# Kernel tuning notes

Hardware: AMD Instinct MI355X
Metric: run time of the kernel (lower is better)

The kernel has to match this reference:

```python
import jax, jax.numpy as jnp
import numpy as np

B, S, D, H, F = 2, 2048, 3072, 32, 8192
DH = D // H  # 96
EPS = 1e-5


def setup_inputs() -> dict:
    key = jax.random.key(0)
    ks = jax.random.split(key, 16)
    sd = 0.02
    inp = {
        "hidden_states": jax.random.normal(ks[0], (B, S, D), jnp.float32),
        "ln1_g": jnp.ones((D,), jnp.float32),
        "ln1_b": jnp.zeros((D,), jnp.float32),
        "Wq": jax.random.normal(ks[1], (D, H, DH), jnp.float32) * sd,
        "bq": jnp.zeros((H, DH), jnp.float32),
        "Wk": jax.random.normal(ks[2], (D, H, DH), jnp.float32) * sd,
        "bk": jnp.zeros((H, DH), jnp.float32),
        "Wv": jax.random.normal(ks[3], (D, H, DH), jnp.float32) * sd,
        "bv": jnp.zeros((H, DH), jnp.float32),
        "Wo": jax.random.normal(ks[4], (H, DH, D), jnp.float32) * sd,
        "bo": jnp.zeros((D,), jnp.float32),
        "ln2_g": jnp.ones((D,), jnp.float32),
        "ln2_b": jnp.zeros((D,), jnp.float32),
        "W1": jax.random.normal(ks[5], (D, F), jnp.float32) * sd,
        "b1": jnp.zeros((F,), jnp.float32),
        "W2": jax.random.normal(ks[6], (F, D), jnp.float32) * sd,
        "b2": jnp.zeros((D,), jnp.float32),
    }
    return inp


def _layernorm(x, g, b):
    m = jnp.mean(x, axis=-1, keepdims=True)
    v = jnp.mean(jnp.square(x - m), axis=-1, keepdims=True)
    return (x - m) * jax.lax.rsqrt(v + EPS) * g + b


def reference(hidden_states, ln1_g, ln1_b, Wq, bq, Wk, bk, Wv, bv, Wo, bo,
              ln2_g, ln2_b, W1, b1, W2, b2):
    # --- LN + self-attention + residual ---
    h = _layernorm(hidden_states, ln1_g, ln1_b)  # [B,S,D]
    q = jnp.einsum('bsd,dhk->bshk', h, Wq) + bq  # [B,S,H,DH]
    k = jnp.einsum('bsd,dhk->bshk', h, Wk) + bk
    v = jnp.einsum('bsd,dhk->bshk', h, Wv) + bv
    scale = 1.0 / np.sqrt(DH).astype(np.float32)
    scores = jnp.einsum('bshk,bthk->bhst', q, k) * scale  # [B,H,S,S]
    attn = jax.nn.softmax(scores, axis=-1)
    ctx = jnp.einsum('bhst,bthk->bshk', attn, v)  # [B,S,H,DH]
    attn_out = jnp.einsum('bshk,hkd->bsd', ctx, Wo) + bo
    h1 = hidden_states + attn_out
    # --- LN + MLP + residual ---
    h2 = _layernorm(h1, ln2_g, ln2_b)
    mlp = jax.nn.gelu(h2 @ W1 + b1, approximate=False) @ W2 + b2
    return h1 + mlp
```

## Files before the change

### kernel.cpp

```cpp
#include <hip/hip_runtime.h>
#include <math.h>

#define DEV __device__ __forceinline__

typedef __attribute__((ext_vector_type(8))) __bf16 bfrag;
typedef __attribute__((ext_vector_type(4))) float f4;
typedef __attribute__((ext_vector_type(8))) unsigned short u16x8;
typedef __attribute__((ext_vector_type(4))) unsigned short u16x4;

DEV unsigned short f2bf(float f) {
  __bf16 b = (__bf16)f;
  unsigned short u;
  __builtin_memcpy(&u, &b, 2);
  return u;
}

DEV void gload_lds16(const void* g, void* l) {
  __builtin_amdgcn_global_load_lds((const __attribute__((address_space(1))) void*)g,
                                   (__attribute__((address_space(3))) void*)l, 16, 0, 0);
}

template<int EPI, int OUTBF, int BIASROW>
__global__ __launch_bounds__(256, 2)
void gemm_bt(const unsigned short* __restrict__ A,
             const unsigned short* __restrict__ Bt,
             const float* __restrict__ bias,
             const float* __restrict__ res,
             void* __restrict__ outp,
             int M, int N, int K, int gm, int cm, int cn)
{
  __shared__ unsigned short As[2][128 * 32];
  __shared__ unsigned short Bs[2][128 * 32];
  const int tid = threadIdx.x;
  const int lane = tid & 63;
  const int wid = tid >> 6;
  const int wr = wid >> 1, wc = wid & 1;
  const int l15 = lane & 15, lg = lane >> 4;

  const int xcd = blockIdx.x & 7, bidx = blockIdx.x >> 3;
  const int cgm = gm / cm;
  const int tm = (xcd % cgm) * cm + bidx % cm;
  const int tn = (xcd / cgm) * cn + bidx / cm;
  const long tM = (long)tm * 128;
  const long tN = (long)tn * 128;

  const int c0 = tid, c1 = tid + 256;
  const int r0 = c0 >> 2, k0 = (c0 & 3) * 8;
  const int r1 = c1 >> 2, k1 = (c1 & 3) * 8;

  const unsigned short* A0 = A + (tM + r0) * (long)K + k0;
  const unsigned short* A1 = A + (tM + r1) * (long)K + k1;
  const unsigned short* B0 = Bt + (tN + r0) * (long)K + k0;
  const unsigned short* B1 = Bt + (tN + r1) * (long)K + k1;

  auto stage = [&](int kt, int buf) {
    const long ko = (long)kt * 32;
    gload_lds16(A0 + ko, &As[buf][c0 * 8]);
    gload_lds16(A1 + ko, &As[buf][c1 * 8]);
    gload_lds16(B0 + ko, &Bs[buf][c0 * 8]);
    gload_lds16(B1 + ko, &Bs[buf][c1 * 8]);
  };

  stage(0, 0);
  f4 acc[4][4] = {};
  const int nk = K >> 5;
  int cur = 0;
  __syncthreads();
  for (int kt = 0; kt < nk; ++kt) {
    if (kt + 1 < nk) stage(kt + 1, cur ^ 1);
    bfrag aF[4], bF[4];
#pragma unroll
    for (int m = 0; m < 4; ++m)
      aF[m] = *(const bfrag*)&As[cur][(wr * 64 + m * 16 + l15) * 32 + lg * 8];
#pragma unroll
    for (int n = 0; n < 4; ++n)
      bF[n] = *(const bfrag*)&Bs[cur][(wc * 64 + n * 16 + l15) * 32 + lg * 8];
#pragma unroll
    for (int m = 0; m < 4; ++m)
#pragma unroll
      for (int n = 0; n < 4; ++n)
        acc[m][n] = __builtin_amdgcn_mfma_f32_16x16x32_bf16(aF[m], bF[n], acc[m][n], 0, 0, 0);
    __syncthreads();
    cur ^= 1;
  }

#pragma unroll
  for (int m = 0; m < 4; ++m) {
#pragma unroll
    for (int n = 0; n < 4; ++n) {
      const long col = tN + wc * 64 + n * 16 + l15;
      const float bcol = BIASROW ? 0.f : bias[col];
#pragma unroll
      for (int e = 0; e < 4; ++e) {
        const long row = tM + wr * 64 + m * 16 + lg * 4 + e;
        float v = acc[m][n][e] + (BIASROW ? bias[row] : bcol);
        if constexpr (EPI == 1) v = 0.5f * v * (1.0f + erff(v * 0.70710678118654752f));
        if constexpr (EPI == 2) v += res[row * N + col];
        if constexpr (OUTBF) ((unsigned short*)outp)[row * N + col] = f2bf(v);
        else                 ((float*)outp)[row * N + col] = v;
      }
    }
  }
}

template<int EPI, int OUTBF, int BIASROW>
__global__ __launch_bounds__(512, 2)
void gemm256(const unsigned short* __restrict__ A,
             const unsigned short* __restrict__ Bt,
             const float* __restrict__ bias,
             const float* __restrict__ res,
             void* __restrict__ outp,
             int M, int N, int K, int gm, int cm, int cn)
{
  __shared__ unsigned short As[2][256 * 64];
  __shared__ unsigned short Bs[2][256 * 64];

  const int tid = threadIdx.x;
  const int lane = tid & 63;
  const int wid = tid >> 6;
  const int wm = wid >> 2, wn = wid & 3;
  const int l15 = lane & 15, lg = lane >> 4;

  const int xcd = blockIdx.x & 7, bidx = blockIdx.x >> 3;
  const int cgm = gm / cm;
  const int tm = (xcd % cgm) * cm + bidx % cm;
  const int tn = (xcd / cgm) * cn + bidx / cm;
  const long tM = (long)tm * 256, tN = (long)tn * 256;

  const int srow = tid >> 3;
  const int lslot = (tid & 7) ^ (srow & 7);
  const unsigned short* aSrc = A + (tM + srow) * (long)K + lslot * 8;
  const unsigned short* bSrc = Bt + (tN + srow) * (long)K + lslot * 8;
  const int NT = K >> 6;

  auto stA = [&](int t, int j) {
    gload_lds16(aSrc + (long)t * 64 + (long)j * 64 * K, &As[t & 1][j * 4096 + tid * 8]);
  };
  auto stB = [&](int t, int j) {
    gload_lds16(bSrc + (long)t * 64 + (long)j * 64 * K, &Bs[t & 1][j * 4096 + tid * 8]);
  };

#pragma unroll
  for (int j = 0; j < 4; ++j) stA(0, j);
#pragma unroll
  for (int j = 0; j < 4; ++j) stB(0, j);
  stA(1, 0); stA(1, 2);
#pragma unroll
  for (int j = 0; j < 4; ++j) stB(1, j);
  asm volatile("s_waitcnt vmcnt(6)" ::: "memory");
  __builtin_amdgcn_s_barrier();

  const int aRow = (wm * 128 + l15) * 64;
  const int bRow = (wn * 64 + l15) * 64;
  const int sx = l15 & 7;
  const int sl0 = ((0 + lg) ^ sx) * 8;
  const int sl1 = ((4 + lg) ^ sx) * 8;

  bfrag aL[4][2], aH[4][2], b01[2][2], b23[2][2];
  f4 acc[8][4] = {};

  int cur = 0;
  for (int t = 0; t < NT; ++t, cur ^= 1) {
    const unsigned short* Ac = As[cur];
    const unsigned short* Bc = Bs[cur];
    const bool s1 = (t + 1 < NT);
    const bool s2 = (t + 2 < NT);

#pragma unroll
    for (int m = 0; m < 4; ++m) {
      aL[m][0] = *(const bfrag*)&Ac[aRow + m * 1024 + sl0];
      aL[m][1] = *(const bfrag*)&Ac[aRow + m * 1024 + sl1];
    }
#pragma unroll
    for (int n = 0; n < 2; ++n) {
      b01[n][0] = *(const bfrag*)&Bc[bRow + n * 1024 + sl0];
      b01[n][1] = *(const bfrag*)&Bc[bRow + n * 1024 + sl1];
    }
#pragma unroll
    for (int n = 0; n < 2; ++n) {
      b23[n][0] = *(const bfrag*)&Bc[bRow + (n + 2) * 1024 + sl0];
      b23[n][1] = *(const bfrag*)&Bc[bRow + (n + 2) * 1024 + sl1];
    }
    if (s1) { stA(t + 1, 1); stA(t + 1, 3); }
    __builtin_amdgcn_s_barrier();
    __builtin_amdgcn_s_setprio(1);
#pragma unroll
    for (int m = 0; m < 4; ++m)
#pragma unroll
      for (int n = 0; n < 2; ++n) {
        acc[m][n] = __builtin_amdgcn_mfma_f32_16x16x32_bf16(aL[m][0], b01[n][0], acc[m][n], 0, 0, 0);
        acc[m][n] = __builtin_amdgcn_mfma_f32_16x16x32_bf16(aL[m][1], b01[n][1], acc[m][n], 0, 0, 0);
      }
    __builtin_amdgcn_s_setprio(0);
    __builtin_amdgcn_s_barrier();

#pragma unroll
    for (int m = 0; m < 4; ++m) {
      aH[m][0] = *(const bfrag*)&Ac[aRow + 4096 + m * 1024 + sl0];
      aH[m][1] = *(const bfrag*)&Ac[aRow + 4096 + m * 1024 + sl1];
    }
    if (s2) { stA(t + 2, 0); stA(t + 2, 2); }
    __builtin_amdgcn_s_barrier();
    __builtin_amdgcn_s_setprio(1);
#pragma unroll
    for (int m = 0; m < 4; ++m)
#pragma unroll
      for (int n = 0; n < 2; ++n) {
        acc[m][2 + n] = __builtin_amdgcn_mfma_f32_16x16x32_bf16(aL[m][0], b23[n][0], acc[m][2 + n], 0, 0, 0);
        acc[m][2 + n] = __builtin_amdgcn_mfma_f32_16x16x32_bf16(aL[m][1], b23[n][1], acc[m][2 + n], 0, 0, 0);
      }
    __builtin_amdgcn_s_setprio(0);
    __builtin_amdgcn_s_barrier();

    if (s2) { stB(t + 2, 0); stB(t + 2, 1); }
    __builtin_amdgcn_s_barrier();
    __builtin_amdgcn_s_setprio(1);
#pragma unroll
    for (int m = 0; m < 4; ++m)
#pragma unroll
      for (int n = 0; n < 2; ++n) {
        acc[4 + m][2 + n] = __builtin_amdgcn_mfma_f32_16x16x32_bf16(aH[m][0], b23[n][0], acc[4 + m][2 + n], 0, 0, 0);
        acc[4 + m][2 + n] = __builtin_amdgcn_mfma_f32_16x16x32_bf16(aH[m][1], b23[n][1], acc[4 + m][2 + n], 0, 0, 0);
      }
    __builtin_amdgcn_s_setprio(0);
    __builtin_amdgcn_s_barrier();

    if (s2) { stB(t + 2, 2); stB(t + 2, 3); }
    __builtin_amdgcn_s_setprio(1);
#pragma unroll
    for (int m = 0; m < 4; ++m)
#pragma unroll
      for (int n = 0; n < 2; ++n) {
        acc[4 + m][n] = __builtin_amdgcn_mfma_f32_16x16x32_bf16(aH[m][0], b01[n][0], acc[4 + m][n], 0, 0, 0);
        acc[4 + m][n] = __builtin_amdgcn_mfma_f32_16x16x32_bf16(aH[m][1], b01[n][1], acc[4 + m][n], 0, 0, 0);
      }
    __builtin_amdgcn_s_setprio(0);
    if (s2)      asm volatile("s_waitcnt vmcnt(6)" ::: "memory");
    else if (s1) asm volatile("s_waitcnt vmcnt(0)" ::: "memory");
    __builtin_amdgcn_s_barrier();
  }

#pragma unroll
  for (int m = 0; m < 8; ++m) {
    const long row0 = tM + wm * 128 + m * 16 + lg * 4;
#pragma unroll
    for (int n = 0; n < 4; ++n) {
      const long col = tN + wn * 64 + n * 16 + l15;
      const float bc = BIASROW ? 0.f : bias[col];
#pragma unroll
      for (int e = 0; e < 4; ++e) {
        const long row = row0 + e;
        float v = acc[m][n][e] + (BIASROW ? bias[row] : bc);
        if constexpr (EPI == 1) v = 0.5f * v * (1.0f + erff(v * 0.70710678118654752f));
        if constexpr (EPI == 2) v += res[row * N + col];
        if constexpr (OUTBF) ((unsigned short*)outp)[row * N + col] = f2bf(v);
        else                 ((float*)outp)[row * N + col] = v;
      }
    }
  }
}

__global__ __launch_bounds__(256)
void ln_bf16(const float* __restrict__ x, const float* __restrict__ g,
             const float* __restrict__ b, unsigned short* __restrict__ out)
{
  __shared__ float red[4];
  const int tid = threadIdx.x;
  const long row = blockIdx.x;
  const float* xr = x + row * 3072;
  float4 v[3];
  float s = 0.f;
#pragma unroll
  for (int i = 0; i < 3; ++i) {
    v[i] = *(const float4*)&xr[i * 1024 + tid * 4];
    s += v[i].x + v[i].y + v[i].z + v[i].w;
  }
#pragma unroll
  for (int o = 32; o > 0; o >>= 1) s += __shfl_xor(s, o);
  if ((tid & 63) == 0) red[tid >> 6] = s;
  __syncthreads();
  s = red[0] + red[1] + red[2] + red[3];
  const float mean = s * (1.f / 3072.f);
  float vs = 0.f;
#pragma unroll
  for (int i = 0; i < 3; ++i) {
    const float dx = v[i].x - mean, dy = v[i].y - mean;
    const float dz = v[i].z - mean, dw = v[i].w - mean;
    vs += dx * dx + dy * dy + dz * dz + dw * dw;
  }
#pragma unroll
  for (int o = 32; o > 0; o >>= 1) vs += __shfl_xor(vs, o);
  __syncthreads();
  if ((tid & 63) == 0) red[tid >> 6] = vs;
  __syncthreads();
  vs = red[0] + red[1] + red[2] + red[3];
  const float rstd = rsqrtf(vs * (1.f / 3072.f) + 1e-5f);
#pragma unroll
  for (int i = 0; i < 3; ++i) {
    const int idx = i * 1024 + tid * 4;
    const float* vp = (const float*)&v[i];
    u16x4 o4;
#pragma unroll
    for (int c = 0; c < 4; ++c)
      o4[c] = f2bf((vp[c] - mean) * rstd * g[idx + c] + b[idx + c]);
    *(u16x4*)&out[row * 3072 + idx] = o4;
  }
}

__global__ __launch_bounds__(256)
void prep_weights(const float* __restrict__ Wq, const float* __restrict__ Wk,
                  const float* __restrict__ Wv, const float* __restrict__ Wo,
                  const float* __restrict__ W1, const float* __restrict__ W2,
                  const float* __restrict__ bq, const float* __restrict__ bk,
                  unsigned short* __restrict__ WqkT, unsigned short* __restrict__ WvT,
                  unsigned short* __restrict__ WoT, unsigned short* __restrict__ W1T,
                  unsigned short* __restrict__ W2T, float* __restrict__ bqk)
{
  __shared__ float tile[64][65];
  const int tid = threadIdx.x;
  int bid = blockIdx.x;
  if (bid < 24) {
    const int i = bid * 256 + tid;
    bqk[i] = (i < 3072) ? bq[i] : bk[i - 3072];
    return;
  }
  bid -= 24;
  const float* in; unsigned short* out; int R, C, nbx;
  if (bid < 2304)       { in = Wq; out = WqkT;               R = 3072; C = 3072; nbx = 48; }
  else if (bid < 4608)  { in = Wk; out = WqkT + 3072 * 3072; R = 3072; C = 3072; nbx = 48; bid -= 2304; }
  else if (bid < 6912)  { in = Wv; out = WvT;                R = 3072; C = 3072; nbx = 48; bid -= 4608; }
  else if (bid < 9216)  { in = Wo; out = WoT;                R = 3072; C = 3072; nbx = 48; bid -= 6912; }
  else if (bid < 15360) { in = W1; out = W1T;                R = 3072; C = 8192; nbx = 128; bid -= 9216; }
  else                  { in = W2; out = W2T;                R = 8192; C = 3072; nbx = 48; bid -= 15360; }
  const int bx = bid % nbx, by = bid / nbx;
  const long r0 = (long)by * 64, c0 = (long)bx * 64;
  const int tr = tid >> 4;
  const int tc = (tid & 15) * 4;

#pragma unroll
  for (int p = 0; p < 4; ++p) {
    const int row = p * 16 + tr;
    const float4 v = *(const float4*)&in[(r0 + row) * C + c0 + tc];
    tile[row][tc + 0] = v.x; tile[row][tc + 1] = v.y;
    tile[row][tc + 2] = v.z; tile[row][tc + 3] = v.w;
  }
  __syncthreads();

#pragma unroll
  for (int q = 0; q < 4; ++q) {
    const int c = q * 16 + tr;
    u16x4 o4;
#pragma unroll
    for (int j = 0; j < 4; ++j)
      o4[j] = f2bf(tile[tc + j][c]);
    *(u16x4*)&out[(c0 + c) * R + r0 + tc] = o4;
  }
}

__global__ __launch_bounds__(256, 4)
void attn_fwd(const unsigned short* __restrict__ qk,
              const unsigned short* __restrict__ vT,
              unsigned short* __restrict__ ctx)
{
  __shared__ unsigned short Ks[64 * 104];
  __shared__ unsigned short Vt[96 * 72];
  __shared__ unsigned short Ps[4 * 16 * 72];
  const int tid = threadIdx.x;
  const int lane = tid & 63;
  const int w = tid >> 6;
  const int l15 = lane & 15, lg = lane >> 4;
  const int bid = (blockIdx.x & 7) * 256 + (blockIdx.x >> 3);
  const int qb = bid & 31;
  const int h = (bid >> 5) & 31;
  const int b = bid >> 10;
  const long qkbase = ((long)b * 2048) * 6144 + h * 96;
  const long obase  = ((long)b * 2048) * 3072 + h * 96;
  const long vbase  = (long)(h * 96) * 4096 + (long)b * 2048;
  const int qbase = qb * 64;

  bfrag qf[3];
#pragma unroll
  for (int ks = 0; ks < 3; ++ks)
    qf[ks] = *(const bfrag*)&qk[qkbase + (long)(qbase + w * 16 + l15) * 6144 + ks * 32 + lg * 8];

  const int kr0 = tid / 12,         kk0 = (tid % 12) * 8;
  const int kr1 = (tid + 256) / 12, kk1 = ((tid + 256) % 12) * 8;
  const int kr2 = (tid + 512) / 12, kk2 = ((tid + 512) % 12) * 8;
  const unsigned short* kg = qk + qkbase + 3072;
  const int vd0 = tid >> 3,           vk0 = (tid & 7) * 8;
  const int vd1 = (tid + 256) >> 3,   vk1 = ((tid + 256) & 7) * 8;
  const int vd2 = (tid + 512) >> 3,   vk2 = ((tid + 512) & 7) * 8;
  const unsigned short* vg = vT + vbase;

  u16x8 kA = *(const u16x8*)&kg[(long)kr0 * 6144 + kk0];
  u16x8 kB = *(const u16x8*)&kg[(long)kr1 * 6144 + kk1];
  u16x8 kC = *(const u16x8*)&kg[(long)kr2 * 6144 + kk2];
  u16x8 vA = *(const u16x8*)&vg[(long)vd0 * 4096 + vk0];
  u16x8 vB = *(const u16x8*)&vg[(long)vd1 * 4096 + vk1];
  u16x8 vC = *(const u16x8*)&vg[(long)vd2 * 4096 + vk2];

  float m_run = -1e30f, l_run = 0.f;
  f4 O[6] = {};
  const float sc = 0.1020620726f * 1.4426950409f;

  for (int t = 0; t < 32; ++t) {
    *(u16x8*)&Ks[kr0 * 104 + kk0] = kA;
    *(u16x8*)&Ks[kr1 * 104 + kk1] = kB;
    *(u16x8*)&Ks[kr2 * 104 + kk2] = kC;
    *(u16x8*)&Vt[vd0 * 72 + vk0] = vA;
    *(u16x8*)&Vt[vd1 * 72 + vk1] = vB;
    *(u16x8*)&Vt[vd2 * 72 + vk2] = vC;
    __syncthreads();
    if (t + 1 < 32) {
      const long ko = (long)(t + 1) * 64 * 6144;
      const long vo = (long)(t + 1) * 64;
      kA = *(const u16x8*)&kg[ko + (long)kr0 * 6144 + kk0];
      kB = *(const u16x8*)&kg[ko + (long)kr1 * 6144 + kk1];
      kC = *(const u16x8*)&kg[ko + (long)kr2 * 6144 + kk2];
      vA = *(const u16x8*)&vg[vo + (long)vd0 * 4096 + vk0];
      vB = *(const u16x8*)&vg[vo + (long)vd1 * 4096 + vk1];
      vC = *(const u16x8*)&vg[vo + (long)vd2 * 4096 + vk2];
    }

    f4 sf[4];
#pragma unroll
    for (int mb = 0; mb < 4; ++mb) {
      f4 z = {0.f, 0.f, 0.f, 0.f};
      sf[mb] = z;
#pragma unroll
      for (int ks = 0; ks < 3; ++ks) {
        bfrag kf = *(const bfrag*)&Ks[(mb * 16 + l15) * 104 + ks * 32 + lg * 8];
        sf[mb] = __builtin_amdgcn_mfma_f32_16x16x32_bf16(kf, qf[ks], sf[mb], 0, 0, 0);
      }
    }
    float p[16];
    float tmax = -1e30f;
#pragma unroll
    for (int mb = 0; mb < 4; ++mb)
#pragma unroll
      for (int e = 0; e < 4; ++e) {
        const float sv = sf[mb][e] * sc;
        p[mb * 4 + e] = sv;
        tmax = fmaxf(tmax, sv);
      }
    tmax = fmaxf(tmax, __shfl_xor(tmax, 16));
    tmax = fmaxf(tmax, __shfl_xor(tmax, 32));
    const bool noskip = !__all(tmax - m_run <= 8.0f);
    float mnew = m_run, alpha = 1.0f;
    if (noskip) {
      mnew = fmaxf(m_run, tmax);
      alpha = exp2f(m_run - mnew);
    }
    float psum = 0.f;
#pragma unroll
    for (int i = 0; i < 16; ++i) {
      p[i] = exp2f(p[i] - mnew);
      psum += p[i];
    }
    psum += __shfl_xor(psum, 16);
    psum += __shfl_xor(psum, 32);
    l_run = l_run * alpha + psum;
    m_run = mnew;
#pragma unroll
    for (int mb = 0; mb < 4; ++mb) {
      u16x4 pw;
#pragma unroll
      for (int e = 0; e < 4; ++e) pw[e] = f2bf(p[mb * 4 + e]);
      *(u16x4*)&Ps[w * 1152 + l15 * 72 + mb * 16 + lg * 4] = pw;
    }
    if (noskip) {
      float aE[4];
#pragma unroll
      for (int e = 0; e < 4; ++e) aE[e] = __shfl(alpha, lg * 4 + e);
#pragma unroll
      for (int nb = 0; nb < 6; ++nb)
#pragma unroll
        for (int e = 0; e < 4; ++e) O[nb][e] *= aE[e];
    }
    bfrag pf[2];
#pragma unroll
    for (int ks = 0; ks < 2; ++ks)
      pf[ks] = *(const bfrag*)&Ps[w * 1152 + l15 * 72 + ks * 32 + lg * 8];
#pragma unroll
    for (int nb = 0; nb < 6; ++nb)
#pragma unroll
      for (int ks = 0; ks < 2; ++ks) {
        bfrag vf = *(const bfrag*)&Vt[(nb * 16 + l15) * 72 + ks * 32 + lg * 8];
        O[nb] = __builtin_amdgcn_mfma_f32_16x16x32_bf16(pf[ks], vf, O[nb], 0, 0, 0);
      }
    __syncthreads();
  }
  float lE[4];
#pragma unroll
  for (int e = 0; e < 4; ++e) lE[e] = 1.f / __shfl(l_run, lg * 4 + e);
#pragma unroll
  for (int nb = 0; nb < 6; ++nb)
#pragma unroll
    for (int e = 0; e < 4; ++e) {
      const long row = qbase + w * 16 + lg * 4 + e;
      ctx[obase + row * 3072 + nb * 16 + l15] = f2bf(O[nb][e] * lE[e]);
    }
}

extern "C" void kernel_launch(void* const* d_in, const int* in_sizes, int n_in,
                              void* d_out, int out_size, void* d_ws, size_t ws_size,
                              hipStream_t stream)
{
  (void)in_sizes; (void)n_in; (void)out_size; (void)ws_size;
  const float* x    = (const float*)d_in[0];
  const float* ln1g = (const float*)d_in[1];
  const float* ln1b = (const float*)d_in[2];
  const float* Wq   = (const float*)d_in[3];
  const float* bq   = (const float*)d_in[4];
  const float* Wk   = (const float*)d_in[5];
  const float* bk   = (const float*)d_in[6];
  const float* Wv   = (const float*)d_in[7];
  const float* bv   = (const float*)d_in[8];
  const float* Wo   = (const float*)d_in[9];
  const float* bo   = (const float*)d_in[10];
  const float* ln2g = (const float*)d_in[11];
  const float* ln2b = (const float*)d_in[12];
  const float* W1   = (const float*)d_in[13];
  const float* b1   = (const float*)d_in[14];
  const float* W2   = (const float*)d_in[15];
  const float* b2   = (const float*)d_in[16];

  char* ws = (char*)d_ws;
  unsigned short* WqkT = (unsigned short*)(ws + 0);
  unsigned short* WvT  = (unsigned short*)(ws + 37748736);
  unsigned short* WoT  = (unsigned short*)(ws + 56623104);
  unsigned short* W1T  = (unsigned short*)(ws + 75497472);
  unsigned short* W2T  = (unsigned short*)(ws + 125829120);
  float*          bqk  = (float*)(ws + 176160768);
  unsigned short* hbf  = (unsigned short*)(ws + 176185344);
  unsigned short* ctxb = hbf;
  unsigned short* qkb  = (unsigned short*)(ws + 201351168);
  unsigned short* h2   = qkb;
  unsigned short* act  = (unsigned short*)(ws + 251682816);
  unsigned short* vTb  = (unsigned short*)(ws + 318791680);
  float*          h1   = (float*)d_out;

  const dim3 blk(256);
  const dim3 blk512(512);

  prep_weights<<<24 + 21504, blk, 0, stream>>>(Wq, Wk, Wv, Wo, W1, W2, bq, bk,
                                               WqkT, WvT, WoT, W1T, W2T, bqk);

  ln_bf16<<<4096, blk, 0, stream>>>(x, ln1g, ln1b, hbf);

  gemm256<0, 1, 0><<<384, blk512, 0, stream>>>(hbf, WqkT, bqk, nullptr, qkb, 4096, 6144, 3072, 16, 8, 6);
  gemm256<0, 1, 1><<<192, blk512, 0, stream>>>(WvT, hbf, bv, nullptr, vTb, 3072, 4096, 3072, 12, 6, 4);

  attn_fwd<<<2048, blk, 0, stream>>>(qkb, vTb, ctxb);

  gemm256<2, 0, 0><<<192, blk512, 0, stream>>>(ctxb, WoT, bo, x, h1, 4096, 3072, 3072, 16, 4, 6);

  ln_bf16<<<4096, blk, 0, stream>>>(h1, ln2g, ln2b, h2);

  gemm256<1, 1, 0><<<512, blk512, 0, stream>>>(h2, W1T, b1, nullptr, act, 4096, 8192, 3072, 16, 8, 8);
  gemm_bt<2, 0, 0><<<768, blk, 0, stream>>>(act, W2T, b2, h1, (float*)d_out, 4096, 3072, 8192, 32, 16, 6);
}
```

Baseline: 1.168 ms.

## Split K in two for the W2 GEMM and accumulate with atomics

The final MLP down-projection GEMM (K=8192) now splits K across two halves of a doubled grid. Each half accumulates into the fp32 output with atomicAdd, and only the first half adds the bias. The launch-bounds occupancy hint for this kernel rises from 2 to 4 blocks per CU. The aim is more parallel work and better latency hiding on a long-K GEMM, at the cost of atomic traffic. The residual is no longer added explicitly, so correctness depends on the output buffer already holding h1.

```diff
diff --git a/kernel.cpp b/kernel.cpp
--- a/kernel.cpp
+++ b/kernel.cpp
@@ -21,13 +21,13 @@
 }
 
 template<int EPI, int OUTBF, int BIASROW>
-__global__ __launch_bounds__(256, 2)
+__global__ __launch_bounds__(256, 4)
 void gemm_bt(const unsigned short* __restrict__ A,
              const unsigned short* __restrict__ Bt,
              const float* __restrict__ bias,
              const float* __restrict__ res,
              void* __restrict__ outp,
-             int M, int N, int K, int gm, int cm, int cn)
+             int M, int N, int K, int gm, int cm, int cn, int nsplit)
 {
   __shared__ unsigned short As[2][128 * 32];
   __shared__ unsigned short Bs[2][128 * 32];
@@ -37,7 +37,13 @@
   const int wr = wid >> 1, wc = wid & 1;
   const int l15 = lane & 15, lg = lane >> 4;
 
-  const int xcd = blockIdx.x & 7, bidx = blockIdx.x >> 3;
+  const int half = gridDim.x >> 1;
+  const int kh = (nsplit == 2 && (int)blockIdx.x >= half) ? 1 : 0;
+  const int bxid = blockIdx.x - kh * half;
+  const int ksub = K / nsplit;
+  const long koff = (long)kh * ksub;
+
+  const int xcd = bxid & 7, bidx = bxid >> 3;
   const int cgm = gm / cm;
   const int tm = (xcd % cgm) * cm + bidx % cm;
   const int tn = (xcd / cgm) * cn + bidx / cm;
@@ -48,10 +54,10 @@
   const int r0 = c0 >> 2, k0 = (c0 & 3) * 8;
   const int r1 = c1 >> 2, k1 = (c1 & 3) * 8;
 
-  const unsigned short* A0 = A + (tM + r0) * (long)K + k0;
-  const unsigned short* A1 = A + (tM + r1) * (long)K + k1;
-  const unsigned short* B0 = Bt + (tN + r0) * (long)K + k0;
-  const unsigned short* B1 = Bt + (tN + r1) * (long)K + k1;
+  const unsigned short* A0 = A + (tM + r0) * (long)K + koff + k0;
+  const unsigned short* A1 = A + (tM + r1) * (long)K + koff + k1;
+  const unsigned short* B0 = Bt + (tN + r0) * (long)K + koff + k0;
+  const unsigned short* B1 = Bt + (tN + r1) * (long)K + koff + k1;
 
   auto stage = [&](int kt, int buf) {
     const long ko = (long)kt * 32;
@@ -63,7 +69,7 @@
 
   stage(0, 0);
   f4 acc[4][4] = {};
-  const int nk = K >> 5;
+  const int nk = ksub >> 5;
   int cur = 0;
   __syncthreads();
   for (int kt = 0; kt < nk; ++kt) {
@@ -93,11 +99,17 @@
 #pragma unroll
       for (int e = 0; e < 4; ++e) {
         const long row = tM + wr * 64 + m * 16 + lg * 4 + e;
-        float v = acc[m][n][e] + (BIASROW ? bias[row] : bcol);
-        if constexpr (EPI == 1) v = 0.5f * v * (1.0f + erff(v * 0.70710678118654752f));
-        if constexpr (EPI == 2) v += res[row * N + col];
-        if constexpr (OUTBF) ((unsigned short*)outp)[row * N + col] = f2bf(v);
-        else                 ((float*)outp)[row * N + col] = v;
+        float v = acc[m][n][e];
+        if constexpr (EPI == 3) {
+          if (kh == 0) v += (BIASROW ? bias[row] : bcol);
+          atomicAdd(&((float*)outp)[row * N + col], v);
+        } else {
+          v += (BIASROW ? bias[row] : bcol);
+          if constexpr (EPI == 1) v = 0.5f * v * (1.0f + erff(v * 0.70710678118654752f));
+          if constexpr (EPI == 2) v += res[row * N + col];
+          if constexpr (OUTBF) ((unsigned short*)outp)[row * N + col] = f2bf(v);
+          else                 ((float*)outp)[row * N + col] = v;
+        }
       }
     }
   }
@@ -558,5 +570,6 @@
   ln_bf16<<<4096, blk, 0, stream>>>(h1, ln2g, ln2b, h2);
 
   gemm256<1, 1, 0><<<512, blk512, 0, stream>>>(h2, W1T, b1, nullptr, act, 4096, 8192, 3072, 16, 8, 8);
-  gemm_bt<2, 0, 0><<<768, blk, 0, stream>>>(act, W2T, b2, h1, (float*)d_out, 4096, 3072, 8192, 32, 16, 6);
-}
+  gemm_bt<3, 0, 0><<<1536, blk, 0, stream>>>(act, W2T, b2, nullptr, (float*)d_out,
+                                             4096, 3072, 8192, 32, 16, 6, 2);
+}
```

Measured after the change: 1.212 ms. 1.04x slower.

## Double attention query tile to 128 rows with 512-thread blocks

Applied to the files above, without the earlier changes.

The attention kernel now processes 128 query rows per block using 8 waves instead of 64 rows with 4 waves, halving the grid. Each K/V tile loaded into shared memory is reused by twice as many query rows, which halves global K/V traffic. Load work is redistributed so 512 threads cover the 768 chunks, with only half the threads doing a second load. Larger blocks may reduce occupancy and make the wave distribution across CUs less even.

```diff
diff --git a/kernel.cpp b/kernel.cpp
--- a/kernel.cpp
+++ b/kernel.cpp
@@ -357,69 +357,70 @@
   }
 }
 
-__global__ __launch_bounds__(256, 4)
+__global__ __launch_bounds__(512, 4)
 void attn_fwd(const unsigned short* __restrict__ qk,
               const unsigned short* __restrict__ vT,
               unsigned short* __restrict__ ctx)
 {
   __shared__ unsigned short Ks[64 * 104];
   __shared__ unsigned short Vt[96 * 72];
-  __shared__ unsigned short Ps[4 * 16 * 72];
+  __shared__ unsigned short Ps[8 * 16 * 72];
   const int tid = threadIdx.x;
   const int lane = tid & 63;
   const int w = tid >> 6;
   const int l15 = lane & 15, lg = lane >> 4;
-  const int bid = (blockIdx.x & 7) * 256 + (blockIdx.x >> 3);
-  const int qb = bid & 31;
-  const int h = (bid >> 5) & 31;
-  const int b = bid >> 10;
+  const int bid = (blockIdx.x & 7) * 128 + (blockIdx.x >> 3);
+  const int qb = bid & 15;
+  const int h = (bid >> 4) & 31;
+  const int b = bid >> 9;
   const long qkbase = ((long)b * 2048) * 6144 + h * 96;
   const long obase  = ((long)b * 2048) * 3072 + h * 96;
   const long vbase  = (long)(h * 96) * 4096 + (long)b * 2048;
-  const int qbase = qb * 64;
+  const int qbase = qb * 128;
 
   bfrag qf[3];
 #pragma unroll
   for (int ks = 0; ks < 3; ++ks)
     qf[ks] = *(const bfrag*)&qk[qkbase + (long)(qbase + w * 16 + l15) * 6144 + ks * 32 + lg * 8];
 
-  const int kr0 = tid / 12,         kk0 = (tid % 12) * 8;
-  const int kr1 = (tid + 256) / 12, kk1 = ((tid + 256) % 12) * 8;
-  const int kr2 = (tid + 512) / 12, kk2 = ((tid + 512) % 12) * 8;
+  const bool two = (w < 4);
+  const int kcA = tid, kcB = tid + 512;
+  const int krA = kcA / 12, kkA = (kcA % 12) * 8;
+  const int krB = kcB / 12, kkB = (kcB % 12) * 8;
   const unsigned short* kg = qk + qkbase + 3072;
-  const int vd0 = tid >> 3,           vk0 = (tid & 7) * 8;
-  const int vd1 = (tid + 256) >> 3,   vk1 = ((tid + 256) & 7) * 8;
-  const int vd2 = (tid + 512) >> 3,   vk2 = ((tid + 512) & 7) * 8;
+  const int vdA = kcA >> 3, vkA = (kcA & 7) * 8;
+  const int vdB = kcB >> 3, vkB = (kcB & 7) * 8;
   const unsigned short* vg = vT + vbase;
 
-  u16x8 kA = *(const u16x8*)&kg[(long)kr0 * 6144 + kk0];
-  u16x8 kB = *(const u16x8*)&kg[(long)kr1 * 6144 + kk1];
-  u16x8 kC = *(const u16x8*)&kg[(long)kr2 * 6144 + kk2];
-  u16x8 vA = *(const u16x8*)&vg[(long)vd0 * 4096 + vk0];
-  u16x8 vB = *(const u16x8*)&vg[(long)vd1 * 4096 + vk1];
-  u16x8 vC = *(const u16x8*)&vg[(long)vd2 * 4096 + vk2];
+  u16x8 kA = *(const u16x8*)&kg[(long)krA * 6144 + kkA];
+  u16x8 vA = *(const u16x8*)&vg[(long)vdA * 4096 + vkA];
+  u16x8 kB, vB;
+  if (two) {
+    kB = *(const u16x8*)&kg[(long)krB * 6144 + kkB];
+    vB = *(const u16x8*)&vg[(long)vdB * 4096 + vkB];
+  }
 
   float m_run = -1e30f, l_run = 0.f;
   f4 O[6] = {};
   const float sc = 0.1020620726f * 1.4426950409f;
 
   for (int t = 0; t < 32; ++t) {
-    *(u16x8*)&Ks[kr0 * 104 + kk0] = kA;
-    *(u16x8*)&Ks[kr1 * 104 + kk1] = kB;
-    *(u16x8*)&Ks[kr2 * 104 + kk2] = kC;
-    *(u16x8*)&Vt[vd0 * 72 + vk0] = vA;
-    *(u16x8*)&Vt[vd1 * 72 + vk1] = vB;
-    *(u16x8*)&Vt[vd2 * 72 + vk2] = vC;
+    *(u16x8*)&Ks[krA * 104 + kkA] = kA;
+    *(u16x8*)&Vt[vdA * 72 + vkA] = vA;
+    if (two) {
+      *(u16x8*)&Ks[krB * 104 + kkB] = kB;
+      *(u16x8*)&Vt[vdB * 72 + vkB] = vB;
+    }
     __syncthreads();
     if (t + 1 < 32) {
       const long ko = (long)(t + 1) * 64 * 6144;
       const long vo = (long)(t + 1) * 64;
-      kA = *(const u16x8*)&kg[ko + (long)kr0 * 6144 + kk0];
-      kB = *(const u16x8*)&kg[ko + (long)kr1 * 6144 + kk1];
-      kC = *(const u16x8*)&kg[ko + (long)kr2 * 6144 + kk2];
-      vA = *(const u16x8*)&vg[vo + (long)vd0 * 4096 + vk0];
-      vB = *(const u16x8*)&vg[vo + (long)vd1 * 4096 + vk1];
-      vC = *(const u16x8*)&vg[vo + (long)vd2 * 4096 + vk2];
+      kA = *(const u16x8*)&kg[ko + (long)krA * 6144 + kkA];
+      vA = *(const u16x8*)&vg[vo + (long)vdA * 4096 + vkA];
+      if (two) {
+        kB = *(const u16x8*)&kg[ko + (long)krB * 6144 + kkB];
+        vB = *(const u16x8*)&vg[vo + (long)vdB * 4096 + vkB];
+      }
     }
 
     f4 sf[4];
@@ -551,7 +552,7 @@
   gemm256<0, 1, 0><<<384, blk512, 0, stream>>>(hbf, WqkT, bqk, nullptr, qkb, 4096, 6144, 3072, 16, 8, 6);
   gemm256<0, 1, 1><<<192, blk512, 0, stream>>>(WvT, hbf, bv, nullptr, vTb, 3072, 4096, 3072, 12, 6, 4);
 
-  attn_fwd<<<2048, blk, 0, stream>>>(qkb, vTb, ctxb);
+  attn_fwd<<<1024, blk512, 0, stream>>>(qkb, vTb, ctxb);
 
   gemm256<2, 0, 0><<<192, blk512, 0, stream>>>(ctxb, WoT, bo, x, h1, 4096, 3072, 3072, 16, 4, 6);
 
```

Result: no change. 1.157 ms (-0.9%).
